# Kernel optimization log

Hardware: AMD Instinct MI355X
Metric: run time of the kernel (lower is better)

The kernel has to match this reference:

```python
import jax, jax.numpy as jnp
import numpy as np

N = 768           # atoms
C = 128           # channels (layer_dims = [128]*4)
A = 8             # atom types
RBF = 4
RBF_LOW, RBF_HIGH = 0.0, 2.5
EPS = 1e-12

# Levi-Civita tensor for the 1x1->1 tensor product
_E = np.zeros((3, 3, 3), np.float32)
_E[0, 1, 2] = _E[1, 2, 0] = _E[2, 0, 1] = 1.0
_E[0, 2, 1] = _E[2, 1, 0] = _E[1, 0, 2] = -1.0
EIJK = jnp.asarray(_E)


def setup_inputs() -> dict:
    key = jax.random.key(0)
    ks = jax.random.split(key, 16)
    r = jax.random.normal(ks[0], (N, 3), jnp.float32) * 2.0
    one_hot = jax.nn.one_hot(jax.random.randint(ks[1], (N,), 0, A), A, dtype=jnp.float32)

    def W(k, shape, fan_in):
        return jax.random.normal(k, shape, jnp.float32) / np.sqrt(fan_in).astype(np.float32)

    return dict(
        r=r, one_hot=one_hot,
        embed_W=W(ks[2], (C, A), A), embed_b=jnp.zeros((C,), jnp.float32),
        # 12 radial nets: layer0 uses ids 0-1, layer1 ids 2-6, layer2 ids 7-11
        Rw1=W(ks[3], (12, RBF, C), RBF), Rb1=jnp.zeros((12, C), jnp.float32),
        Rw2=W(ks[4], (12, C, C), C), Rb2=jnp.zeros((12, C), jnp.float32),
        si0_w0=W(ks[5], (C, C), C), si0_b0=jnp.zeros((C,), jnp.float32),
        si0_w1=W(ks[6], (C, C), C),
        si1_w0=W(ks[7], (C, 2 * C), 2 * C), si1_b0=jnp.zeros((C,), jnp.float32),
        si1_w1=W(ks[8], (C, 3 * C), 3 * C),
        si2_w0=W(ks[9], (C, 2 * C), 2 * C), si2_b0=jnp.zeros((C,), jnp.float32),
        si2_w1=W(ks[10], (C, 3 * C), 3 * C),
        nl_b0=jnp.zeros((C,), jnp.float32), nl_b1=jnp.zeros((C,), jnp.float32),
        pred_W=W(ks[11], (A, C), C), pred_b=jnp.zeros((A,), jnp.float32),
    )


def _gated(x, b):
    # norm-gated equivariant nonlinearity for l=1 features [N, C, 3]
    n = jnp.sqrt(jnp.maximum(jnp.sum(x * x, -1), EPS))
    return x * (jax.nn.elu(b[None, :] + n) / n)[..., None]


def reference(r, one_hot, embed_W, embed_b, Rw1, Rb1, Rw2, Rb2,
              si0_w0, si0_b0, si0_w1, si1_w0, si1_b0, si1_w1,
              si2_w0, si2_b0, si2_w1, nl_b0, nl_b1, pred_W, pred_b):
    rij = r[:, None, :] - r[None, :, :]                     # [N,N,3]
    dij = jnp.sqrt(jnp.maximum(jnp.sum(rij * rij, -1), EPS))  # [N,N]
    u = rij / (dij[..., None] + 1e-8)                        # unit vectors
    centers = jnp.linspace(RBF_LOW, RBF_HIGH, RBF)
    gamma = RBF / (RBF_HIGH - RBF_LOW)                       # 1 / spacing
    rbf = jnp.exp(-gamma * jnp.square(dij[..., None] - centers))  # [N,N,RBF]

    def radial(i):  # per-filter radial net on rbf features -> [N,N,C]
        h = jax.nn.relu(jnp.einsum('abr,rc->abc', rbf, Rw1[i]) + Rb1[i])
        return jnp.einsum('abc,cd->abd', h, Rw2[i]) + Rb2[i]

    def si(x, w, b=None):  # self-interaction linear over channel dim f
        y = jnp.einsum('afm,gf->agm', x, w)
        return y if b is None else y + b[:, None]

    e = (one_hot @ embed_W.T + embed_b)[..., None]           # [N,C,1]

    # layer 0: only an l=0 input exists
    c00 = jnp.einsum('abf,bfm->afm', radial(0), e)                 # 0x0->0
    c01 = jnp.einsum('abf,abi,bf->afi', radial(1), u, e[..., 0])   # 0x1->1
    x0 = jax.nn.elu(si(c00, si0_w0, si0_b0))
    x1 = _gated(si(c01, si0_w1), nl_b0)

    def full_layer(x0, x1, ri, w0, b0, w1):
        a0 = jnp.einsum('abf,bfm->afm', radial(ri), x0)                        # 0x0->0
        b1 = jnp.einsum('abf,abi,bf->afi', radial(ri + 1), u, x0[..., 0])      # 0x1->1
        a1 = jnp.einsum('abf,bfm->afm', radial(ri + 2), x1)                    # 1x0->1
        o0 = jnp.einsum('abf,abj,bfj->af', radial(ri + 3), u, x1)[..., None]   # 1x1->0
        o1 = jnp.einsum('ijk,abf,abj,bfk->afi', EIJK, radial(ri + 4), u, x1)   # 1x1->1
        y0 = si(jnp.concatenate([a0, o0], 1), w0, b0)   # [N,2C,1] -> [N,C,1]
        y1 = si(jnp.concatenate([b1, a1, o1], 1), w1)   # [N,3C,3] -> [N,C,3]
        return y0, y1

    x0, x1 = full_layer(x0, x1, 2, si1_w0, si1_b0, si1_w1)
    x0, x1 = jax.nn.elu(x0), _gated(x1, nl_b1)
    x0, x1 = full_layer(x0, x1, 7, si2_w0, si2_b0, si2_w1)  # last layer: no nonlinearity

    atom = (x0[..., 0] @ pred_W.T + pred_b)[..., None]      # [N,A,1]
    # (probability_scalars, missing_coordinates, atom_type_scalars)
    return x0, x1, atom
```

## Files before the change

### kernel.cpp

```cpp
#include <hip/hip_runtime.h>
#include <hip/hip_fp16.h>
#include <math.h>


constexpr int   N_    = 768;
constexpr int   C_    = 128;
constexpr int   M_    = 320;
constexpr float DMAX_ = 6.4f;
constexpr float GAMMA_ = 1.6f;

__global__ __launch_bounds__(256) void build_table_kernel(
    const float* __restrict__ Rw1, const float* __restrict__ Rb1,
    const float* __restrict__ Rw2, const float* __restrict__ Rb2,
    __half2* __restrict__ tab, float delta)
{
    const int f  = threadIdx.x & 127, fh = threadIdx.x >> 7;
    const int m0 = blockIdx.x * 4;

    __shared__ float hs[2][5][C_];

    float rbf[5][4];
    const float cent[4] = {0.0f, 2.5f / 3.0f, 5.0f / 3.0f, 2.5f};
#pragma unroll
    for (int mm = 0; mm < 5; ++mm) {
        int m = m0 + mm; if (m > M_ - 1) m = M_ - 1;
        const float d = (float)m * delta;
#pragma unroll
        for (int k = 0; k < 4; ++k) {
            const float t = d - cent[k];
            rbf[mm][k] = expf(-GAMMA_ * t * t);
        }
    }

    for (int ii = 0; ii < 6; ++ii) {
        const int i = fh * 6 + ii;
        float w1v[4];
#pragma unroll
        for (int k = 0; k < 4; ++k) w1v[k] = Rw1[(i * 4 + k) * C_ + f];
        const float b1v = Rb1[i * C_ + f];

        __syncthreads();
#pragma unroll
        for (int mm = 0; mm < 5; ++mm) {
            float acc = b1v;
#pragma unroll
            for (int k = 0; k < 4; ++k) acc = fmaf(rbf[mm][k], w1v[k], acc);
            hs[fh][mm][f] = fmaxf(acc, 0.0f);
        }
        __syncthreads();

        const float b2v = Rb2[i * C_ + f];
        float out[5] = {b2v, b2v, b2v, b2v, b2v};
        for (int c = 0; c < C_; ++c) {
            const float w = Rw2[(i * C_ + c) * C_ + f];
#pragma unroll
            for (int mm = 0; mm < 5; ++mm) out[mm] = fmaf(hs[fh][mm][c], w, out[mm]);
        }
#pragma unroll
        for (int mm = 0; mm < 4; ++mm) {
            const int m = m0 + mm;
            if (m < M_)
                tab[((size_t)m * 12 + i) * C_ + f] =
                    __floats2half2_rn(out[mm], out[mm + 1] - out[mm]);
        }
    }
}

__global__ __launch_bounds__(256) void embed_kernel(
    const float* __restrict__ onehot, const float* __restrict__ eW,
    const float* __restrict__ eb, float* __restrict__ e)
{
    const int idx = blockIdx.x * 256 + threadIdx.x;
    const int b = idx >> 7, f = idx & 127;
    float acc = eb[f];
#pragma unroll
    for (int t = 0; t < 8; ++t) acc = fmaf(onehot[b * 8 + t], eW[f * 8 + t], acc);
    e[idx] = acc;
}

template <int RI>
__device__ inline void pair_setup(const float* __restrict__ r, int a, int bbase,
                                  int tid, float4* pair, int* qoff)
{
    const float rax = r[a * 3 + 0], ray = r[a * 3 + 1], raz = r[a * 3 + 2];
    for (int i = tid; i < 384; i += 256) {
        const int b = bbase + i;
        const float dx = rax - r[b * 3 + 0];
        const float dy = ray - r[b * 3 + 1];
        const float dz = raz - r[b * 3 + 2];
        const float d2 = fmaf(dx, dx, fmaf(dy, dy, dz * dz));
        const float d  = sqrtf(fmaxf(d2, 1e-12f));
        const float inv = 1.0f / (d + 1e-8f);
        const float t = d * ((float)(M_ - 1) / DMAX_);
        int q = (int)t; q = q > M_ - 2 ? M_ - 2 : q;
        const float fr = fminf(t - (float)q, 1.0f);
        pair[i] = make_float4(dx * inv, dy * inv, dz * inv, fr);
        qoff[i] = (q * 12 + RI) * C_;
    }
}

__global__ __launch_bounds__(256, 8) void pair0_kernel(
    const float* __restrict__ r, const float* __restrict__ e,
    const __half2* __restrict__ tab, float* __restrict__ P)
{
    const int a = blockIdx.x >> 1, p = blockIdx.x & 1;
    const int tid = threadIdx.x;
    const int f = tid & 127, part = tid >> 7;
    const int bbase = p * 384;

    __shared__ float4 pair[384];
    __shared__ int    qoff[384];
    __shared__ float  sred[4][2][C_];

    pair_setup<0>(r, a, bbase, tid, pair, qoff);
    __syncthreads();

    float c00 = 0.f, cx = 0.f, cy = 0.f, cz = 0.f;
    const __half2* tabf = tab + f;
    const int iBeg = part * 192, iEnd = iBeg + 192;
    for (int i = iBeg; i < iEnd; ++i) {
        const float4 pr = pair[i];
        const __half2* tp = tabf + qoff[i];
        const __half2 h0 = tp[0], h1 = tp[C_];
        const float eb_ = e[(bbase + i) * C_ + f];
        const float fr = pr.w;
        const float2 v0 = __half22float2(h0);
        const float2 v1 = __half22float2(h1);
        const float t0 = fmaf(fr, v0.y, v0.x);
        const float t1 = fmaf(fr, v1.y, v1.x);
        c00 = fmaf(t0, eb_, c00);
        const float te = t1 * eb_;
        cx = fmaf(te, pr.x, cx); cy = fmaf(te, pr.y, cy); cz = fmaf(te, pr.z, cz);
    }

    sred[0][part][f] = c00;
    sred[1][part][f] = cx;
    sred[2][part][f] = cy;
    sred[3][part][f] = cz;
    __syncthreads();

    for (int idx = tid; idx < 4 * C_; idx += 256) {
        const int k = idx >> 7, c = idx & 127;
        P[((size_t)(p * N_ + a) * 4 + k) * C_ + c] =
            sred[k][0][c] + sred[k][1][c];
    }
}

template <int RI>
__global__ __launch_bounds__(256, 8) void pairF_kernel(
    const float* __restrict__ r, const uint2* __restrict__ xin,
    const __half2* __restrict__ tab, float* __restrict__ P)
{
    const int a = blockIdx.x >> 1, p = blockIdx.x & 1;
    const int tid = threadIdx.x;
    const int f = tid & 127, part = tid >> 7;
    const int bbase = p * 384;

    __shared__ float4 pair[384];
    __shared__ int    qoff[384];
    __shared__ float  sred[11][2][C_];

    pair_setup<RI>(r, a, bbase, tid, pair, qoff);
    __syncthreads();

    float a0 = 0.f, b1x = 0.f, b1y = 0.f, b1z = 0.f;
    float a1x = 0.f, a1y = 0.f, a1z = 0.f;
    float o0 = 0.f, o1x = 0.f, o1y = 0.f, o1z = 0.f;

    const __half2* tabf = tab + f;
    const uint2*   xf   = xin + (size_t)bbase * C_ + f;
    const int iBeg = part * 192, iEnd = iBeg + 192;
    for (int i = iBeg; i < iEnd; ++i) {
        const float4 pr = pair[i];
        const __half2* tp = tabf + qoff[i];
        const __half2 h0 = tp[0 * C_], h1 = tp[1 * C_], h2 = tp[2 * C_];
        const __half2 h3 = tp[3 * C_], h4 = tp[4 * C_];
        const uint2 xw = xf[(size_t)i * C_];

        const float fr = pr.w;
        const float2 v0 = __half22float2(h0);
        const float2 v1 = __half22float2(h1);
        const float2 v2 = __half22float2(h2);
        const float2 v3 = __half22float2(h3);
        const float2 v4 = __half22float2(h4);
        const float t0 = fmaf(fr, v0.y, v0.x);
        const float t1 = fmaf(fr, v1.y, v1.x);
        const float t2 = fmaf(fr, v2.y, v2.x);
        const float t3 = fmaf(fr, v3.y, v3.x);
        const float t4 = fmaf(fr, v4.y, v4.x);

        const float2 x01 = __half22float2(*(const __half2*)&xw.x);
        const float2 x23 = __half22float2(*(const __half2*)&xw.y);
        const float x0b = x01.x, xbx = x01.y, xby = x23.x, xbz = x23.y;

        a0 = fmaf(t0, x0b, a0);
        const float tb = t1 * x0b;
        b1x = fmaf(tb, pr.x, b1x); b1y = fmaf(tb, pr.y, b1y); b1z = fmaf(tb, pr.z, b1z);
        a1x = fmaf(t2, xbx, a1x); a1y = fmaf(t2, xby, a1y); a1z = fmaf(t2, xbz, a1z);
        const float ud = fmaf(pr.x, xbx, fmaf(pr.y, xby, pr.z * xbz));
        o0 = fmaf(t3, ud, o0);
        const float crx = pr.y * xbz - pr.z * xby;
        const float cry = pr.z * xbx - pr.x * xbz;
        const float crz = pr.x * xby - pr.y * xbx;
        o1x = fmaf(t4, crx, o1x); o1y = fmaf(t4, cry, o1y); o1z = fmaf(t4, crz, o1z);
    }

    sred[0][part][f] = a0;
    sred[1][part][f] = b1x; sred[2][part][f] = b1y; sred[3][part][f] = b1z;
    sred[4][part][f] = a1x; sred[5][part][f] = a1y; sred[6][part][f] = a1z;
    sred[7][part][f] = o0;
    sred[8][part][f] = o1x; sred[9][part][f] = o1y; sred[10][part][f] = o1z;
    __syncthreads();

    for (int idx = tid; idx < 11 * C_; idx += 256) {
        const int k = idx >> 7, c = idx & 127;
        P[((size_t)(p * N_ + a) * 11 + k) * C_ + c] =
            sred[k][0][c] + sred[k][1][c];
    }
}

__global__ __launch_bounds__(512) void finish0_kernel(
    const float* __restrict__ P,
    const float* __restrict__ w0, const float* __restrict__ b0v,
    const float* __restrict__ w1, const float* __restrict__ nlb,
    uint2* __restrict__ xout)
{
    const int a = blockIdx.x, tid = threadIdx.x;
    const int f = tid & 127;

    __shared__ float s[4 * C_];
    __shared__ float ys[4 * C_];

    for (int idx = tid; idx < 4 * C_; idx += 512)
        s[idx] = P[(size_t)a * 4 * C_ + idx] +
                 P[((size_t)(N_ + a) * 4) * C_ + idx];
    __syncthreads();

    {
        const int j = tid >> 7;
        float y;
        if (j == 0) {
            y = b0v[f];
            const float4* w = (const float4*)(w0 + (size_t)f * C_);
            for (int c4 = 0; c4 < C_ / 4; ++c4) {
                const float4 wv = w[c4];
                y = fmaf(wv.x, s[c4 * 4 + 0], y);
                y = fmaf(wv.y, s[c4 * 4 + 1], y);
                y = fmaf(wv.z, s[c4 * 4 + 2], y);
                y = fmaf(wv.w, s[c4 * 4 + 3], y);
            }
        } else {
            y = 0.f;
            const float4* w = (const float4*)(w1 + (size_t)f * C_);
            const float* sj = s + j * C_;
            for (int c4 = 0; c4 < C_ / 4; ++c4) {
                const float4 wv = w[c4];
                y = fmaf(wv.x, sj[c4 * 4 + 0], y);
                y = fmaf(wv.y, sj[c4 * 4 + 1], y);
                y = fmaf(wv.z, sj[c4 * 4 + 2], y);
                y = fmaf(wv.w, sj[c4 * 4 + 3], y);
            }
        }
        ys[j * C_ + f] = y;
    }
    __syncthreads();

    if (tid < C_) {
        const float y0 = ys[tid];
        const float yx = ys[C_ + tid], yy = ys[2 * C_ + tid], yz = ys[3 * C_ + tid];
        const float x0v = y0 > 0.f ? y0 : expm1f(y0);
        const float nsq = fmaf(yx, yx, fmaf(yy, yy, yz * yz));
        const float nn  = sqrtf(fmaxf(nsq, 1e-12f));
        const float g   = nlb[tid] + nn;
        const float sc  = (g > 0.f ? g : expm1f(g)) / nn;
        uint2 w;
        *(__half2*)&w.x = __floats2half2_rn(x0v, yx * sc);
        *(__half2*)&w.y = __floats2half2_rn(yy * sc, yz * sc);
        xout[(size_t)a * C_ + tid] = w;
    }
}

template <bool NONLIN, bool LAST>
__global__ __launch_bounds__(512) void finishF_kernel(
    const float* __restrict__ P,
    const float* __restrict__ w0, const float* __restrict__ b0v,
    const float* __restrict__ w1, const float* __restrict__ nlb,
    uint2* __restrict__ xout,
    float* __restrict__ out, const float* __restrict__ predW,
    const float* __restrict__ predb)
{
    const int a = blockIdx.x, tid = threadIdx.x;
    const int f = tid & 127;

    __shared__ float s[11 * C_];
    __shared__ float ys[4 * C_];

    for (int idx = tid; idx < 11 * C_; idx += 512)
        s[idx] = P[(size_t)a * 11 * C_ + idx] +
                 P[((size_t)(N_ + a) * 11) * C_ + idx];
    __syncthreads();

    {
        const int j = tid >> 7;
        float y;
        if (j == 0) {
            y = b0v[f];
            const float4* w = (const float4*)(w0 + (size_t)f * (2 * C_));
            const float* s0 = s + 0 * C_;
            const float* s7 = s + 7 * C_;
            for (int c4 = 0; c4 < C_ / 4; ++c4) {
                const float4 wa = w[c4];
                const float4 wb = w[C_ / 4 + c4];
                y = fmaf(wa.x, s0[c4 * 4 + 0], y);
                y = fmaf(wa.y, s0[c4 * 4 + 1], y);
                y = fmaf(wa.z, s0[c4 * 4 + 2], y);
                y = fmaf(wa.w, s0[c4 * 4 + 3], y);
                y = fmaf(wb.x, s7[c4 * 4 + 0], y);
                y = fmaf(wb.y, s7[c4 * 4 + 1], y);
                y = fmaf(wb.z, s7[c4 * 4 + 2], y);
                y = fmaf(wb.w, s7[c4 * 4 + 3], y);
            }
        } else {
            y = 0.f;
            const float4* w = (const float4*)(w1 + (size_t)f * (3 * C_));
            const float* sb = s + j * C_;
            const float* sa = s + (3 + j) * C_;
            const float* so = s + (7 + j) * C_;
            for (int c4 = 0; c4 < C_ / 4; ++c4) {
                const float4 w_b = w[c4];
                const float4 w_a = w[C_ / 4 + c4];
                const float4 w_o = w[2 * (C_ / 4) + c4];
                y = fmaf(w_b.x, sb[c4 * 4 + 0], y);
                y = fmaf(w_b.y, sb[c4 * 4 + 1], y);
                y = fmaf(w_b.z, sb[c4 * 4 + 2], y);
                y = fmaf(w_b.w, sb[c4 * 4 + 3], y);
                y = fmaf(w_a.x, sa[c4 * 4 + 0], y);
                y = fmaf(w_a.y, sa[c4 * 4 + 1], y);
                y = fmaf(w_a.z, sa[c4 * 4 + 2], y);
                y = fmaf(w_a.w, sa[c4 * 4 + 3], y);
                y = fmaf(w_o.x, so[c4 * 4 + 0], y);
                y = fmaf(w_o.y, so[c4 * 4 + 1], y);
                y = fmaf(w_o.z, so[c4 * 4 + 2], y);
                y = fmaf(w_o.w, so[c4 * 4 + 3], y);
            }
        }
        ys[j * C_ + f] = y;
    }
    __syncthreads();

    if (NONLIN) {
        if (tid < C_) {
            const float y0 = ys[tid];
            const float yx = ys[C_ + tid], yy = ys[2 * C_ + tid], yz = ys[3 * C_ + tid];
            const float x0v = y0 > 0.f ? y0 : expm1f(y0);
            const float nsq = fmaf(yx, yx, fmaf(yy, yy, yz * yz));
            const float nn  = sqrtf(fmaxf(nsq, 1e-12f));
            const float g   = nlb[tid] + nn;
            const float sc  = (g > 0.f ? g : expm1f(g)) / nn;
            uint2 w;
            *(__half2*)&w.x = __floats2half2_rn(x0v, yx * sc);
            *(__half2*)&w.y = __floats2half2_rn(yy * sc, yz * sc);
            xout[(size_t)a * C_ + tid] = w;
        }
    }
    if (LAST) {
        if (tid < C_) {
            const float y0 = ys[tid];
            const float yx = ys[C_ + tid], yy = ys[2 * C_ + tid], yz = ys[3 * C_ + tid];
            out[a * C_ + tid] = y0;
            float* o1 = out + N_ * C_;
            o1[a * (C_ * 3) + tid * 3 + 0] = yx;
            o1[a * (C_ * 3) + tid * 3 + 1] = yy;
            o1[a * (C_ * 3) + tid * 3 + 2] = yz;
        }
        __syncthreads();
        if (tid < 8) {
            float acc = predb[tid];
            for (int c = 0; c < C_; ++c)
                acc = fmaf(predW[tid * C_ + c], ys[c], acc);
            out[N_ * C_ + N_ * C_ * 3 + a * 8 + tid] = acc;
        }
    }
}

extern "C" void kernel_launch(void* const* d_in, const int* in_sizes, int n_in,
                              void* d_out, int out_size, void* d_ws, size_t ws_size,
                              hipStream_t stream)
{
    const float* r       = (const float*)d_in[0];
    const float* onehot  = (const float*)d_in[1];
    const float* embed_W = (const float*)d_in[2];
    const float* embed_b = (const float*)d_in[3];
    const float* Rw1     = (const float*)d_in[4];
    const float* Rb1     = (const float*)d_in[5];
    const float* Rw2     = (const float*)d_in[6];
    const float* Rb2     = (const float*)d_in[7];
    const float* si0_w0  = (const float*)d_in[8];
    const float* si0_b0  = (const float*)d_in[9];
    const float* si0_w1  = (const float*)d_in[10];
    const float* si1_w0  = (const float*)d_in[11];
    const float* si1_b0  = (const float*)d_in[12];
    const float* si1_w1  = (const float*)d_in[13];
    const float* si2_w0  = (const float*)d_in[14];
    const float* si2_b0  = (const float*)d_in[15];
    const float* si2_w1  = (const float*)d_in[16];
    const float* nl_b0   = (const float*)d_in[17];
    const float* nl_b1   = (const float*)d_in[18];
    const float* pred_W  = (const float*)d_in[19];
    const float* pred_b  = (const float*)d_in[20];
    (void)in_sizes; (void)n_in; (void)out_size; (void)ws_size;

    const float delta = DMAX_ / (float)(M_ - 1);

    char* wsb = (char*)d_ws;
    __half2* table = (__half2*)wsb;
    float*   e     = (float*)(wsb + 1966080);
    uint2*   xa    = (uint2*)(wsb + 1966080 + 393216);
    uint2*   xb    = (uint2*)(wsb + 1966080 + 393216 + 786432);
    float*   P     = (float*)(wsb + 1966080 + 393216 + 786432 * 2);

    float* out = (float*)d_out;

    build_table_kernel<<<M_ / 4, 256, 0, stream>>>(Rw1, Rb1, Rw2, Rb2, table, delta);
    embed_kernel<<<(N_ * C_) / 256, 256, 0, stream>>>(onehot, embed_W, embed_b, e);

    pair0_kernel<<<2 * N_, 256, 0, stream>>>(r, e, table, P);
    finish0_kernel<<<N_, 512, 0, stream>>>(P, si0_w0, si0_b0, si0_w1, nl_b0, xa);

    pairF_kernel<2><<<2 * N_, 256, 0, stream>>>(r, xa, table, P);
    finishF_kernel<true, false><<<N_, 512, 0, stream>>>(
        P, si1_w0, si1_b0, si1_w1, nl_b1, xb, nullptr, nullptr, nullptr);

    pairF_kernel<7><<<2 * N_, 256, 0, stream>>>(r, xb, table, P);
    finishF_kernel<false, true><<<N_, 512, 0, stream>>>(
        P, si2_w0, si2_b0, si2_w1, nullptr, nullptr, out, pred_W, pred_b);
}
```

Baseline: 537.5 us.

## Interleave radial lookup table per layer, use packed half2 lerp, widen b-split

The radial-filter lookup table is reorganised into per-layer interleaved tables (tab0, tab1, tab2), so each pair iteration fetches all of its filters with one or two wide vector loads instead of five strided half2 loads. Interpolation now runs in packed half2 FMA, and the table resolution rises to 512 points. The neighbour loop can split four ways across blocks when the workspace is large enough, which gives more blocks and shorter inner loops but more partial sums for the finish kernels to add. The interpolation step loses some precision because it is done in fp16.

```diff
diff --git a/kernel.cpp b/kernel.cpp
--- a/kernel.cpp
+++ b/kernel.cpp
@@ -5,19 +5,28 @@
 
 constexpr int   N_    = 768;
 constexpr int   C_    = 128;
-constexpr int   M_    = 320;
+constexpr int   M_    = 512;
 constexpr float DMAX_ = 6.4f;
 constexpr float GAMMA_ = 1.6f;
+
+__device__ inline unsigned pk2(float a, float b) {
+    __half2 h = __floats2half2_rn(a, b);
+    return *(unsigned*)&h;
+}
 
 __global__ __launch_bounds__(256) void build_table_kernel(
     const float* __restrict__ Rw1, const float* __restrict__ Rb1,
     const float* __restrict__ Rw2, const float* __restrict__ Rb2,
-    __half2* __restrict__ tab, float delta)
+    uint2* __restrict__ tab0, char* __restrict__ tab1, char* __restrict__ tab2,
+    float delta)
 {
     const int f  = threadIdx.x & 127, fh = threadIdx.x >> 7;
     const int m0 = blockIdx.x * 4;
 
     __shared__ float hs[2][5][C_];
+
+    const int filt0[6] = {0, 1, 7, 8, 9, 10};
+    const int filt1[6] = {2, 3, 4, 5, 6, 11};
 
     float rbf[5][4];
     const float cent[4] = {0.0f, 2.5f / 3.0f, 5.0f / 3.0f, 2.5f};
@@ -32,8 +41,10 @@
         }
     }
 
+    float outF[6][5];
+
     for (int ii = 0; ii < 6; ++ii) {
-        const int i = fh * 6 + ii;
+        const int i = fh ? filt1[ii] : filt0[ii];
         float w1v[4];
 #pragma unroll
         for (int k = 0; k < 4; ++k) w1v[k] = Rw1[(i * 4 + k) * C_ + f];
@@ -57,11 +68,33 @@
             for (int mm = 0; mm < 5; ++mm) out[mm] = fmaf(hs[fh][mm][c], w, out[mm]);
         }
 #pragma unroll
-        for (int mm = 0; mm < 4; ++mm) {
-            const int m = m0 + mm;
-            if (m < M_)
-                tab[((size_t)m * 12 + i) * C_ + f] =
-                    __floats2half2_rn(out[mm], out[mm + 1] - out[mm]);
+        for (int mm = 0; mm < 5; ++mm) outF[ii][mm] = out[mm];
+    }
+
+#pragma unroll
+    for (int mm = 0; mm < 4; ++mm) {
+        const int m = m0 + mm;
+        if (m >= M_) continue;
+        float v[6], dl[6];
+#pragma unroll
+        for (int ii = 0; ii < 6; ++ii) {
+            v[ii]  = outF[ii][mm];
+            dl[ii] = outF[ii][mm + 1] - outF[ii][mm];
+        }
+        const size_t eo = (size_t)m * C_ + f;
+        if (fh == 0) {
+            tab0[eo] = make_uint2(pk2(v[0], v[1]), pk2(dl[0], dl[1]));
+            uint4 w;
+            w.x = pk2(v[2], v[3]); w.y = pk2(dl[2], dl[3]);
+            w.z = pk2(v[4], v[5]); w.w = pk2(dl[4], dl[5]);
+            *(uint4*)(tab2 + eo * 32) = w;
+        } else {
+            uint4 w;
+            w.x = pk2(v[0], v[1]); w.y = pk2(dl[0], dl[1]);
+            w.z = pk2(v[2], v[3]); w.w = pk2(dl[2], dl[3]);
+            *(uint4*)(tab1 + eo * 32) = w;
+            *(uint2*)(tab1 + eo * 32 + 16) = make_uint2(pk2(v[4], 0.f), pk2(dl[4], 0.f));
+            *(uint2*)(tab2 + eo * 32 + 16) = make_uint2(pk2(v[5], 0.f), pk2(dl[5], 0.f));
         }
     }
 }
@@ -78,12 +111,12 @@
     e[idx] = acc;
 }
 
-template <int RI>
 __device__ inline void pair_setup(const float* __restrict__ r, int a, int bbase,
-                                  int tid, float4* pair, int* qoff)
+                                  int nb, int tid, int qstride,
+                                  float4* pair, int* qoff)
 {
     const float rax = r[a * 3 + 0], ray = r[a * 3 + 1], raz = r[a * 3 + 2];
-    for (int i = tid; i < 384; i += 256) {
+    for (int i = tid; i < nb; i += 256) {
         const int b = bbase + i;
         const float dx = rax - r[b * 3 + 0];
         const float dy = ray - r[b * 3 + 1];
@@ -95,39 +128,38 @@
         int q = (int)t; q = q > M_ - 2 ? M_ - 2 : q;
         const float fr = fminf(t - (float)q, 1.0f);
         pair[i] = make_float4(dx * inv, dy * inv, dz * inv, fr);
-        qoff[i] = (q * 12 + RI) * C_;
+        qoff[i] = q * qstride;
     }
 }
 
 __global__ __launch_bounds__(256, 8) void pair0_kernel(
     const float* __restrict__ r, const float* __restrict__ e,
-    const __half2* __restrict__ tab, float* __restrict__ P)
-{
-    const int a = blockIdx.x >> 1, p = blockIdx.x & 1;
+    const uint2* __restrict__ tab0, float* __restrict__ P, int nsplit)
+{
+    const int a = blockIdx.x / nsplit, p = blockIdx.x - a * nsplit;
     const int tid = threadIdx.x;
     const int f = tid & 127, part = tid >> 7;
-    const int bbase = p * 384;
+    const int nb = N_ / nsplit, bbase = p * nb;
 
     __shared__ float4 pair[384];
     __shared__ int    qoff[384];
     __shared__ float  sred[4][2][C_];
 
-    pair_setup<0>(r, a, bbase, tid, pair, qoff);
+    pair_setup(r, a, bbase, nb, tid, C_ * 8, pair, qoff);
     __syncthreads();
 
     float c00 = 0.f, cx = 0.f, cy = 0.f, cz = 0.f;
-    const __half2* tabf = tab + f;
-    const int iBeg = part * 192, iEnd = iBeg + 192;
+    const char*  tb = (const char*)tab0 + f * 8;
+    const float* ef = e + (size_t)bbase * C_ + f;
+    const int half_nb = nb >> 1;
+    const int iBeg = part * half_nb, iEnd = iBeg + half_nb;
     for (int i = iBeg; i < iEnd; ++i) {
         const float4 pr = pair[i];
-        const __half2* tp = tabf + qoff[i];
-        const __half2 h0 = tp[0], h1 = tp[C_];
-        const float eb_ = e[(bbase + i) * C_ + f];
-        const float fr = pr.w;
-        const float2 v0 = __half22float2(h0);
-        const float2 v1 = __half22float2(h1);
-        const float t0 = fmaf(fr, v0.y, v0.x);
-        const float t1 = fmaf(fr, v1.y, v1.x);
+        const uint2 W = *(const uint2*)(tb + qoff[i]);
+        const float eb_ = ef[(size_t)i * C_];
+        const __half2 fr2 = __float2half2_rn(pr.w);
+        const __half2 t01 = __hfma2(fr2, *(const __half2*)&W.y, *(const __half2*)&W.x);
+        const float t0 = __low2float(t01), t1 = __high2float(t01);
         c00 = fmaf(t0, eb_, c00);
         const float te = t1 * eb_;
         cx = fmaf(te, pr.x, cx); cy = fmaf(te, pr.y, cy); cz = fmaf(te, pr.z, cz);
@@ -141,61 +173,56 @@
 
     for (int idx = tid; idx < 4 * C_; idx += 256) {
         const int k = idx >> 7, c = idx & 127;
-        P[((size_t)(p * N_ + a) * 4 + k) * C_ + c] =
-            sred[k][0][c] + sred[k][1][c];
-    }
-}
-
-template <int RI>
+        P[((size_t)(p * N_ + a) * 4) * C_ + idx] = sred[k][0][c] + sred[k][1][c];
+    }
+}
+
 __global__ __launch_bounds__(256, 8) void pairF_kernel(
     const float* __restrict__ r, const uint2* __restrict__ xin,
-    const __half2* __restrict__ tab, float* __restrict__ P)
-{
-    const int a = blockIdx.x >> 1, p = blockIdx.x & 1;
+    const char* __restrict__ tab, float* __restrict__ P, int nsplit)
+{
+    const int a = blockIdx.x / nsplit, p = blockIdx.x - a * nsplit;
     const int tid = threadIdx.x;
     const int f = tid & 127, part = tid >> 7;
-    const int bbase = p * 384;
+    const int nb = N_ / nsplit, bbase = p * nb;
 
     __shared__ float4 pair[384];
     __shared__ int    qoff[384];
     __shared__ float  sred[11][2][C_];
 
-    pair_setup<RI>(r, a, bbase, tid, pair, qoff);
+    pair_setup(r, a, bbase, nb, tid, C_ * 32, pair, qoff);
     __syncthreads();
 
     float a0 = 0.f, b1x = 0.f, b1y = 0.f, b1z = 0.f;
     float a1x = 0.f, a1y = 0.f, a1z = 0.f;
     float o0 = 0.f, o1x = 0.f, o1y = 0.f, o1z = 0.f;
 
-    const __half2* tabf = tab + f;
-    const uint2*   xf   = xin + (size_t)bbase * C_ + f;
-    const int iBeg = part * 192, iEnd = iBeg + 192;
+    const char*  tb = tab + f * 32;
+    const uint2* xf = xin + (size_t)bbase * C_ + f;
+    const int half_nb = nb >> 1;
+    const int iBeg = part * half_nb, iEnd = iBeg + half_nb;
     for (int i = iBeg; i < iEnd; ++i) {
         const float4 pr = pair[i];
-        const __half2* tp = tabf + qoff[i];
-        const __half2 h0 = tp[0 * C_], h1 = tp[1 * C_], h2 = tp[2 * C_];
-        const __half2 h3 = tp[3 * C_], h4 = tp[4 * C_];
+        const int off = qoff[i];
+        const uint4 Wa = *(const uint4*)(tb + off);
+        const uint2 Wb = *(const uint2*)(tb + off + 16);
         const uint2 xw = xf[(size_t)i * C_];
 
-        const float fr = pr.w;
-        const float2 v0 = __half22float2(h0);
-        const float2 v1 = __half22float2(h1);
-        const float2 v2 = __half22float2(h2);
-        const float2 v3 = __half22float2(h3);
-        const float2 v4 = __half22float2(h4);
-        const float t0 = fmaf(fr, v0.y, v0.x);
-        const float t1 = fmaf(fr, v1.y, v1.x);
-        const float t2 = fmaf(fr, v2.y, v2.x);
-        const float t3 = fmaf(fr, v3.y, v3.x);
-        const float t4 = fmaf(fr, v4.y, v4.x);
+        const __half2 fr2 = __float2half2_rn(pr.w);
+        const __half2 t01 = __hfma2(fr2, *(const __half2*)&Wa.y, *(const __half2*)&Wa.x);
+        const __half2 t23 = __hfma2(fr2, *(const __half2*)&Wa.w, *(const __half2*)&Wa.z);
+        const __half2 t4h = __hfma2(fr2, *(const __half2*)&Wb.y, *(const __half2*)&Wb.x);
+        const float t0 = __low2float(t01), t1 = __high2float(t01);
+        const float t2 = __low2float(t23), t3 = __high2float(t23);
+        const float t4 = __low2float(t4h);
 
         const float2 x01 = __half22float2(*(const __half2*)&xw.x);
         const float2 x23 = __half22float2(*(const __half2*)&xw.y);
         const float x0b = x01.x, xbx = x01.y, xby = x23.x, xbz = x23.y;
 
         a0 = fmaf(t0, x0b, a0);
-        const float tb = t1 * x0b;
-        b1x = fmaf(tb, pr.x, b1x); b1y = fmaf(tb, pr.y, b1y); b1z = fmaf(tb, pr.z, b1z);
+        const float tb_ = t1 * x0b;
+        b1x = fmaf(tb_, pr.x, b1x); b1y = fmaf(tb_, pr.y, b1y); b1z = fmaf(tb_, pr.z, b1z);
         a1x = fmaf(t2, xbx, a1x); a1y = fmaf(t2, xby, a1y); a1z = fmaf(t2, xbz, a1z);
         const float ud = fmaf(pr.x, xbx, fmaf(pr.y, xby, pr.z * xbz));
         o0 = fmaf(t3, ud, o0);
@@ -214,8 +241,7 @@
 
     for (int idx = tid; idx < 11 * C_; idx += 256) {
         const int k = idx >> 7, c = idx & 127;
-        P[((size_t)(p * N_ + a) * 11 + k) * C_ + c] =
-            sred[k][0][c] + sred[k][1][c];
+        P[((size_t)(p * N_ + a) * 11) * C_ + idx] = sred[k][0][c] + sred[k][1][c];
     }
 }
 
@@ -223,7 +249,7 @@
     const float* __restrict__ P,
     const float* __restrict__ w0, const float* __restrict__ b0v,
     const float* __restrict__ w1, const float* __restrict__ nlb,
-    uint2* __restrict__ xout)
+    uint2* __restrict__ xout, int nsplit)
 {
     const int a = blockIdx.x, tid = threadIdx.x;
     const int f = tid & 127;
@@ -231,9 +257,12 @@
     __shared__ float s[4 * C_];
     __shared__ float ys[4 * C_];
 
-    for (int idx = tid; idx < 4 * C_; idx += 512)
-        s[idx] = P[(size_t)a * 4 * C_ + idx] +
-                 P[((size_t)(N_ + a) * 4) * C_ + idx];
+    for (int idx = tid; idx < 4 * C_; idx += 512) {
+        float acc = 0.f;
+        for (int sp = 0; sp < nsplit; ++sp)
+            acc += P[((size_t)(sp * N_ + a) * 4) * C_ + idx];
+        s[idx] = acc;
+    }
     __syncthreads();
 
     {
@@ -287,7 +316,7 @@
     const float* __restrict__ w1, const float* __restrict__ nlb,
     uint2* __restrict__ xout,
     float* __restrict__ out, const float* __restrict__ predW,
-    const float* __restrict__ predb)
+    const float* __restrict__ predb, int nsplit)
 {
     const int a = blockIdx.x, tid = threadIdx.x;
     const int f = tid & 127;
@@ -295,9 +324,12 @@
     __shared__ float s[11 * C_];
     __shared__ float ys[4 * C_];
 
-    for (int idx = tid; idx < 11 * C_; idx += 512)
-        s[idx] = P[(size_t)a * 11 * C_ + idx] +
-                 P[((size_t)(N_ + a) * 11) * C_ + idx];
+    for (int idx = tid; idx < 11 * C_; idx += 512) {
+        float acc = 0.f;
+        for (int sp = 0; sp < nsplit; ++sp)
+            acc += P[((size_t)(sp * N_ + a) * 11) * C_ + idx];
+        s[idx] = acc;
+    }
     __syncthreads();
 
     {
@@ -408,30 +440,38 @@
     const float* nl_b1   = (const float*)d_in[18];
     const float* pred_W  = (const float*)d_in[19];
     const float* pred_b  = (const float*)d_in[20];
-    (void)in_sizes; (void)n_in; (void)out_size; (void)ws_size;
+    (void)in_sizes; (void)n_in; (void)out_size;
 
     const float delta = DMAX_ / (float)(M_ - 1);
 
     char* wsb = (char*)d_ws;
-    __half2* table = (__half2*)wsb;
-    float*   e     = (float*)(wsb + 1966080);
-    uint2*   xa    = (uint2*)(wsb + 1966080 + 393216);
-    uint2*   xb    = (uint2*)(wsb + 1966080 + 393216 + 786432);
-    float*   P     = (float*)(wsb + 1966080 + 393216 + 786432 * 2);
+    size_t off = 0;
+    char*  tab1 = wsb + off; off += (size_t)M_ * C_ * 32;
+    char*  tab2 = wsb + off; off += (size_t)M_ * C_ * 32;
+    uint2* tab0 = (uint2*)(wsb + off); off += (size_t)M_ * C_ * 8;
+    float* e    = (float*)(wsb + off); off += (size_t)N_ * C_ * 4;
+    uint2* xa   = (uint2*)(wsb + off); off += (size_t)N_ * C_ * 8;
+    uint2* xb   = (uint2*)(wsb + off); off += (size_t)N_ * C_ * 8;
+    float* P    = (float*)(wsb + off);
+
+    const size_t p4 = 4ull * N_ * 11 * C_ * 4;
+    const int nsplit = (ws_size >= off + p4) ? 4 : 2;
 
     float* out = (float*)d_out;
 
-    build_table_kernel<<<M_ / 4, 256, 0, stream>>>(Rw1, Rb1, Rw2, Rb2, table, delta);
+    build_table_kernel<<<M_ / 4, 256, 0, stream>>>(Rw1, Rb1, Rw2, Rb2,
+                                                   tab0, tab1, tab2, delta);
     embed_kernel<<<(N_ * C_) / 256, 256, 0, stream>>>(onehot, embed_W, embed_b, e);
 
-    pair0_kernel<<<2 * N_, 256, 0, stream>>>(r, e, table, P);
-    finish0_kernel<<<N_, 512, 0, stream>>>(P, si0_w0, si0_b0, si0_w1, nl_b0, xa);
-
-    pairF_kernel<2><<<2 * N_, 256, 0, stream>>>(r, xa, table, P);
+    pair0_kernel<<<nsplit * N_, 256, 0, stream>>>(r, e, tab0, P, nsplit);
+    finish0_kernel<<<N_, 512, 0, stream>>>(P, si0_w0, si0_b0, si0_w1, nl_b0,
+                                           xa, nsplit);
+
+    pairF_kernel<<<nsplit * N_, 256, 0, stream>>>(r, xa, tab1, P, nsplit);
     finishF_kernel<true, false><<<N_, 512, 0, stream>>>(
-        P, si1_w0, si1_b0, si1_w1, nl_b1, xb, nullptr, nullptr, nullptr);
-
-    pairF_kernel<7><<<2 * N_, 256, 0, stream>>>(r, xb, table, P);
+        P, si1_w0, si1_b0, si1_w1, nl_b1, xb, nullptr, nullptr, nullptr, nsplit);
+
+    pairF_kernel<<<nsplit * N_, 256, 0, stream>>>(r, xb, tab2, P, nsplit);
     finishF_kernel<false, true><<<N_, 512, 0, stream>>>(
-        P, si2_w0, si2_b0, si2_w1, nullptr, nullptr, out, pred_W, pred_b);
-}
+        P, si2_w0, si2_b0, si2_w1, nullptr, nullptr, out, pred_W, pred_b, nsplit);
+}
```

Measured after the change: 598.9 us. +11.4%, slower.
